# Kernel optimization log

Hardware: AMD Instinct MI355X
Metric: run time of the kernel (lower is better)

The kernel has to match this reference:

```python
import jax, jax.numpy as jnp
import numpy as np

B, N, E, H, D, FF = 4, 4096, 128, 8, 16, 512
EPS = 1e-6


def rmsnorm(x, w):
    return x * jax.lax.rsqrt(jnp.mean(x * x, axis=-1, keepdims=True) + EPS) * w


def setup_inputs() -> dict:
    key = jax.random.key(0)
    ks = jax.random.split(key, 12)
    s = 1.0 / np.sqrt(E)
    return {
        "x": jax.random.normal(ks[0], (B, N, E), jnp.float32),
        "dis_matrix": jax.random.uniform(ks[1], (B, N, N), jnp.float32),
        "g_in": jnp.ones((E,), jnp.float32),
        "g_post": jnp.ones((E,), jnp.float32),
        "Wq": jax.random.normal(ks[2], (E, E), jnp.float32) * s,
        "Wk": jax.random.normal(ks[3], (E, E), jnp.float32) * s,
        "Wv": jax.random.normal(ks[4], (E, E), jnp.float32) * s,
        "alpha": jnp.float32(1.0),
        "Wo": jax.random.normal(ks[5], (H * D, E), jnp.float32) * s,
        "W1": jax.random.normal(ks[6], (E, FF), jnp.float32) * s,
        "b1": jnp.zeros((FF,), jnp.float32),
        "W2": jax.random.normal(ks[7], (FF, E), jnp.float32) / np.sqrt(FF),
        "b2": jnp.zeros((E,), jnp.float32),
    }


def reference(x, dis_matrix, g_in, g_post, Wq, Wk, Wv, alpha, Wo, W1, b1, W2, b2):
    b, n, e = x.shape
    h = rmsnorm(x, g_in)
    # project and split heads: [B,N,E] -> [B,H,N,D]
    def heads(y):
        return y.reshape(b, n, H, D).transpose(0, 2, 1, 3)
    q = heads(h @ Wq)
    k = heads(h @ Wk)
    v = heads(h @ Wv)
    # distance-decayed kernel weights [B,N,N]
    dis_w = jnp.exp(-alpha * np.log2(n) * dis_matrix)
    kw = jnp.exp(k)  # [B,H,N,D]
    w1 = jnp.einsum('bij,bhik->bhjk', dis_w, kw * v)
    w2 = jnp.einsum('bij,bhik->bhjk', dis_w, kw)
    att = jax.nn.sigmoid(q) * (w1 / w2)  # [B,H,N,D]
    att = att.transpose(0, 2, 1, 3).reshape(b, n, e)
    out1 = x + att @ Wo
    h2 = rmsnorm(out1, g_post)
    ff = jax.nn.relu(h2 @ W1 + b1) @ W2 + b2
    return out1 + ff
```

## Files before the change

### kernel.cpp

```cpp
#include <hip/hip_runtime.h>
#include <stdint.h>


typedef __attribute__((ext_vector_type(8))) short short8;
typedef __attribute__((ext_vector_type(4))) float f32x4;

__device__ __forceinline__ uint16_t f2bf(float f) {
    uint32_t u = __builtin_bit_cast(uint32_t, f);
    u += 0x7fffu + ((u >> 16) & 1u);
    return (uint16_t)(u >> 16);
}
__device__ __forceinline__ float bf2f(uint16_t h) {
    uint32_t u = ((uint32_t)h) << 16;
    return __builtin_bit_cast(float, u);
}
__device__ __forceinline__ f32x4 mfma16(short8 a, short8 b, f32x4 c) {
    return __builtin_amdgcn_mfma_f32_16x16x32_bf16(a, b, c, 0, 0, 0);
}

__global__ __launch_bounds__(256) void k_prep(
    const float* __restrict__ Wq, const float* __restrict__ Wk,
    const float* __restrict__ Wv, const float* __restrict__ Wo,
    const float* __restrict__ W1, const float* __restrict__ W2,
    uint16_t* __restrict__ wqkvT, uint16_t* __restrict__ woT,
    uint16_t* __restrict__ w1T, uint16_t* __restrict__ w2T) {
    int t = blockIdx.x * 256 + threadIdx.x;
    if (t < 49152) {
        int n = t >> 7, k = t & 127;
        const float* W = (n < 128) ? Wq : (n < 256) ? Wk : Wv;
        wqkvT[t] = f2bf(W[k * 128 + (n & 127)]);
    } else if (t < 65536) {
        int i = t - 49152; int e = i >> 7, d = i & 127;
        woT[i] = f2bf(Wo[d * 128 + e]);
    } else if (t < 131072) {
        int i = t - 65536; int f = i >> 7, e = i & 127;
        w1T[i] = f2bf(W1[e * 512 + f]);
    } else if (t < 196608) {
        int i = t - 131072; int e = i >> 9, f = i & 511;
        w2T[i] = f2bf(W2[f * 128 + e]);
    }
}

__global__ __launch_bounds__(256) void k_rms(
    const float* __restrict__ x, const float* __restrict__ g,
    uint16_t* __restrict__ o) {
    int row = blockIdx.x * 4 + (threadIdx.x >> 6);
    int l = threadIdx.x & 63;
    float2 v = *(const float2*)(x + (size_t)row * 128 + l * 2);
    float ss = v.x * v.x + v.y * v.y;
    #pragma unroll
    for (int m = 32; m >= 1; m >>= 1) ss += __shfl_xor(ss, m, 64);
    float rs = rsqrtf(ss * (1.0f / 128.0f) + 1e-6f);
    float2 gv = *(const float2*)(g + l * 2);
    uint32_t lo = (uint32_t)f2bf(v.x * rs * gv.x) |
                  ((uint32_t)f2bf(v.y * rs * gv.y) << 16);
    *(uint32_t*)(o + (size_t)row * 128 + l * 2) = lo;
}

__global__ __launch_bounds__(384) void k_qkv(
    const uint16_t* __restrict__ h, const uint16_t* __restrict__ wqkvT,
    uint16_t* __restrict__ sigq, uint16_t* __restrict__ mcatT) {
    __shared__ __align__(16) char sm[65536];
    uint16_t* Al = (uint16_t*)sm;
    float*    Pl = (float*)sm;
    const int t = threadIdx.x;
    const int i0 = blockIdx.x * 64;
    for (int idx = t; idx < 1024; idx += 384) {
        int row = idx >> 4, c8 = (idx & 15) * 8;
        *(uint4*)&Al[row * 136 + c8] =
            *(const uint4*)(h + (size_t)(i0 + row) * 128 + c8);
    }
    __syncthreads();
    const int w = t >> 6, l = t & 63, ml = l & 15, qd = l >> 4;
    f32x4 acc[4][4];
    f32x4 zv = {0.f, 0.f, 0.f, 0.f};
    #pragma unroll
    for (int a = 0; a < 4; ++a)
        #pragma unroll
        for (int b = 0; b < 4; ++b) acc[a][b] = zv;
    #pragma unroll
    for (int kc = 0; kc < 4; ++kc) {
        short8 af[4], bfr[4];
        #pragma unroll
        for (int fm = 0; fm < 4; ++fm)
            af[fm] = *(const short8*)&Al[(fm * 16 + ml) * 136 + kc * 32 + qd * 8];
        #pragma unroll
        for (int fn = 0; fn < 4; ++fn)
            bfr[fn] = *(const short8*)(wqkvT + (w * 64 + fn * 16 + ml) * 128 + kc * 32 + qd * 8);
        #pragma unroll
        for (int fm = 0; fm < 4; ++fm)
            #pragma unroll
            for (int fn = 0; fn < 4; ++fn)
                acc[fm][fn] = mfma16(af[fm], bfr[fn], acc[fm][fn]);
    }
    __syncthreads();
    const int bb = i0 >> 12, il0 = i0 & 4095;
    if (w < 2) {
        #pragma unroll
        for (int fm = 0; fm < 4; ++fm)
            #pragma unroll
            for (int fn = 0; fn < 4; ++fn)
                #pragma unroll
                for (int r = 0; r < 4; ++r) {
                    int row = fm * 16 + qd * 4 + r;
                    int col = w * 64 + fn * 16 + ml;
                    sigq[(size_t)(i0 + row) * 128 + col] =
                        f2bf(1.f / (1.f + __expf(-acc[fm][fn][r])));
                }
    } else {
        int half = (w < 4) ? 0 : 1;
        int cbase = (w - (half ? 4 : 2)) * 64;
        #pragma unroll
        for (int fm = 0; fm < 4; ++fm)
            #pragma unroll
            for (int fn = 0; fn < 4; ++fn)
                #pragma unroll
                for (int r = 0; r < 4; ++r) {
                    int row = fm * 16 + qd * 4 + r;
                    int col = cbase + fn * 16 + ml;
                    float vv = acc[fm][fn][r];
                    if (!half) vv = __expf(vv);
                    Pl[row * 256 + half * 128 + ((col + row) & 127)] = vv;
                }
    }
    __syncthreads();
    for (int idx = t; idx < 16384; idx += 384) {
        int cc = idx >> 6, il = idx & 63;
        int pc = ((cc & 127) + il) & 127;
        float ekw = Pl[il * 256 + pc];
        float val = (cc < 128) ? ekw * Pl[il * 256 + 128 + pc] : ekw;
        mcatT[((size_t)bb * 256 + cc) * 4096 + il0 + il] = f2bf(val);
    }
}

__global__ __launch_bounds__(512) void k_big(
    const float* __restrict__ dis, const uint16_t* __restrict__ mcatT,
    const float* __restrict__ alpha_p, float* __restrict__ wbuf) {
    __shared__ __align__(16) uint16_t Al[128 * 72];
    __shared__ __align__(16) uint16_t Bl[256 * 72];
    const int t = threadIdx.x;
    const int j0 = blockIdx.x * 128;
    const int b  = blockIdx.y;
    const int sp = blockIdx.z;
    const float c = -12.0f * alpha_p[0];
    const int w = t >> 6, l = t & 63, ml = l & 15, qd = l >> 4;
    const int wm = w >> 2, wn = w & 3;
    const int sj4 = (t & 31) * 4, si0 = (t >> 5) * 4;
    const float* disb = dis + (size_t)b * 4096 * 4096;
    const uint16_t* mb = mcatT + (size_t)b * 256 * 4096;

    f32x4 acc[4][4];
    f32x4 zv = {0.f, 0.f, 0.f, 0.f};
    #pragma unroll
    for (int a = 0; a < 4; ++a)
        #pragma unroll
        for (int q = 0; q < 4; ++q) acc[a][q] = zv;

    for (int ks = 0; ks < 32; ++ks) {
        const int ig = sp * 2048 + ks * 64;
        float dv[4][4];
        #pragma unroll
        for (int r = 0; r < 4; ++r) {
            float4 v = *(const float4*)(disb + (size_t)(ig + si0 + r) * 4096 + j0 + sj4);
            dv[r][0] = v.x; dv[r][1] = v.y; dv[r][2] = v.z; dv[r][3] = v.w;
        }
        __syncthreads();
        #pragma unroll
        for (int jj = 0; jj < 4; ++jj) {
            uint32_t lo = (uint32_t)f2bf(__expf(c * dv[0][jj])) |
                          ((uint32_t)f2bf(__expf(c * dv[1][jj])) << 16);
            uint32_t hi = (uint32_t)f2bf(__expf(c * dv[2][jj])) |
                          ((uint32_t)f2bf(__expf(c * dv[3][jj])) << 16);
            uint2 pk = {lo, hi};
            *(uint2*)&Al[(sj4 + jj) * 72 + si0] = pk;
        }
        #pragma unroll
        for (int ii = 0; ii < 4; ++ii) {
            int idx = t + ii * 512;
            int row = idx >> 3, c8 = (idx & 7) * 8;
            *(uint4*)&Bl[row * 72 + c8] =
                *(const uint4*)(mb + (size_t)row * 4096 + ig + c8);
        }
        __syncthreads();
        #pragma unroll
        for (int kc = 0; kc < 2; ++kc) {
            short8 af[4], bfr[4];
            #pragma unroll
            for (int fm = 0; fm < 4; ++fm)
                af[fm] = *(const short8*)&Al[(wm * 64 + fm * 16 + ml) * 72 + kc * 32 + qd * 8];
            #pragma unroll
            for (int fn = 0; fn < 4; ++fn)
                bfr[fn] = *(const short8*)&Bl[(wn * 64 + fn * 16 + ml) * 72 + kc * 32 + qd * 8];
            #pragma unroll
            for (int fm = 0; fm < 4; ++fm)
                #pragma unroll
                for (int fn = 0; fn < 4; ++fn)
                    acc[fm][fn] = mfma16(af[fm], bfr[fn], acc[fm][fn]);
        }
    }
    float* ob = wbuf + ((size_t)(sp * 4 + b) * 4096 + j0) * 256;
    #pragma unroll
    for (int fm = 0; fm < 4; ++fm)
        #pragma unroll
        for (int fn = 0; fn < 4; ++fn) {
            int col = wn * 64 + fn * 16 + ml;
            #pragma unroll
            for (int r = 0; r < 4; ++r) {
                int rowl = wm * 64 + fm * 16 + qd * 4 + r;
                ob[(size_t)rowl * 256 + col] = acc[fm][fn][r];
            }
        }
}

__global__ __launch_bounds__(256) void k_att(
    const float* __restrict__ wbuf, const uint16_t* __restrict__ sigq,
    const uint16_t* __restrict__ woT, const float* __restrict__ x,
    float* __restrict__ out1) {
    __shared__ __align__(16) uint16_t Al[64 * 136];
    __shared__ __align__(16) uint16_t Bl[128 * 136];
    const int t = threadIdx.x;
    const int i0 = blockIdx.x * 64;
    const int b = i0 >> 12, jl0 = i0 & 4095;
    const float* wb0 = wbuf + ((size_t)b * 4096 + jl0) * 256;
    const float* wb1 = wbuf + ((size_t)(4 + b) * 4096 + jl0) * 256;
    #pragma unroll
    for (int ii = 0; ii < 8; ++ii) {
        int idx = t + ii * 256;
        int row = idx >> 5, c4 = (idx & 31) * 4;
        float4 a0 = *(const float4*)(wb0 + (size_t)row * 256 + c4);
        float4 a1 = *(const float4*)(wb1 + (size_t)row * 256 + c4);
        float4 d0 = *(const float4*)(wb0 + (size_t)row * 256 + 128 + c4);
        float4 d1 = *(const float4*)(wb1 + (size_t)row * 256 + 128 + c4);
        const uint16_t* sq = sigq + (size_t)(i0 + row) * 128 + c4;
        uint32_t lo = (uint32_t)f2bf(bf2f(sq[0]) * (a0.x + a1.x) / (d0.x + d1.x)) |
                      ((uint32_t)f2bf(bf2f(sq[1]) * (a0.y + a1.y) / (d0.y + d1.y)) << 16);
        uint32_t hi = (uint32_t)f2bf(bf2f(sq[2]) * (a0.z + a1.z) / (d0.z + d1.z)) |
                      ((uint32_t)f2bf(bf2f(sq[3]) * (a0.w + a1.w) / (d0.w + d1.w)) << 16);
        uint2 pk = {lo, hi};
        *(uint2*)&Al[row * 136 + c4] = pk;
    }
    #pragma unroll
    for (int ii = 0; ii < 8; ++ii) {
        int idx = t + ii * 256;
        int row = idx >> 4, c8 = (idx & 15) * 8;
        *(uint4*)&Bl[row * 136 + c8] = *(const uint4*)(woT + row * 128 + c8);
    }
    __syncthreads();
    const int w = t >> 6, l = t & 63, ml = l & 15, qd = l >> 4;
    const int wm = w >> 1, wn = w & 1;
    f32x4 acc[2][4];
    f32x4 zv = {0.f, 0.f, 0.f, 0.f};
    #pragma unroll
    for (int a = 0; a < 2; ++a)
        #pragma unroll
        for (int q = 0; q < 4; ++q) acc[a][q] = zv;
    #pragma unroll
    for (int kc = 0; kc < 4; ++kc) {
        short8 af[2], bfr[4];
        #pragma unroll
        for (int fm = 0; fm < 2; ++fm)
            af[fm] = *(const short8*)&Al[(wm * 32 + fm * 16 + ml) * 136 + kc * 32 + qd * 8];
        #pragma unroll
        for (int fn = 0; fn < 4; ++fn)
            bfr[fn] = *(const short8*)&Bl[(wn * 64 + fn * 16 + ml) * 136 + kc * 32 + qd * 8];
        #pragma unroll
        for (int fm = 0; fm < 2; ++fm)
            #pragma unroll
            for (int fn = 0; fn < 4; ++fn)
                acc[fm][fn] = mfma16(af[fm], bfr[fn], acc[fm][fn]);
    }
    #pragma unroll
    for (int fm = 0; fm < 2; ++fm)
        #pragma unroll
        for (int fn = 0; fn < 4; ++fn) {
            int col = wn * 64 + fn * 16 + ml;
            #pragma unroll
            for (int r = 0; r < 4; ++r) {
                int rowl = wm * 32 + fm * 16 + qd * 4 + r;
                size_t o = (size_t)(i0 + rowl) * 128 + col;
                out1[o] = x[o] + acc[fm][fn][r];
            }
        }
}

__global__ __launch_bounds__(256) void k_ff1(
    const uint16_t* __restrict__ h2, const uint16_t* __restrict__ w1T,
    const float* __restrict__ b1, uint16_t* __restrict__ R) {
    __shared__ __align__(16) uint16_t Al[64 * 136];
    __shared__ __align__(16) uint16_t Bl[128 * 136];
    const int t = threadIdx.x;
    const int i0 = blockIdx.x * 64;
    const int nt = blockIdx.y;
    #pragma unroll
    for (int ii = 0; ii < 4; ++ii) {
        int idx = t + ii * 256;
        int row = idx >> 4, c8 = (idx & 15) * 8;
        *(uint4*)&Al[row * 136 + c8] =
            *(const uint4*)(h2 + (size_t)(i0 + row) * 128 + c8);
    }
    #pragma unroll
    for (int ii = 0; ii < 8; ++ii) {
        int idx = t + ii * 256;
        int row = idx >> 4, c8 = (idx & 15) * 8;
        *(uint4*)&Bl[row * 136 + c8] =
            *(const uint4*)(w1T + (size_t)(nt * 128 + row) * 128 + c8);
    }
    __syncthreads();
    const int w = t >> 6, l = t & 63, ml = l & 15, qd = l >> 4;
    const int wm = w >> 1, wn = w & 1;
    f32x4 acc[2][4];
    f32x4 zv = {0.f, 0.f, 0.f, 0.f};
    #pragma unroll
    for (int a = 0; a < 2; ++a)
        #pragma unroll
        for (int q = 0; q < 4; ++q) acc[a][q] = zv;
    #pragma unroll
    for (int kc = 0; kc < 4; ++kc) {
        short8 af[2], bfr[4];
        #pragma unroll
        for (int fm = 0; fm < 2; ++fm)
            af[fm] = *(const short8*)&Al[(wm * 32 + fm * 16 + ml) * 136 + kc * 32 + qd * 8];
        #pragma unroll
        for (int fn = 0; fn < 4; ++fn)
            bfr[fn] = *(const short8*)&Bl[(wn * 64 + fn * 16 + ml) * 136 + kc * 32 + qd * 8];
        #pragma unroll
        for (int fm = 0; fm < 2; ++fm)
            #pragma unroll
            for (int fn = 0; fn < 4; ++fn)
                acc[fm][fn] = mfma16(af[fm], bfr[fn], acc[fm][fn]);
    }
    #pragma unroll
    for (int fm = 0; fm < 2; ++fm)
        #pragma unroll
        for (int fn = 0; fn < 4; ++fn) {
            int col = wn * 64 + fn * 16 + ml;
            int gcol = nt * 128 + col;
            #pragma unroll
            for (int r = 0; r < 4; ++r) {
                int rowl = wm * 32 + fm * 16 + qd * 4 + r;
                R[(size_t)(i0 + rowl) * 512 + gcol] =
                    f2bf(fmaxf(acc[fm][fn][r] + b1[gcol], 0.f));
            }
        }
}

__global__ __launch_bounds__(256) void k_ff2(
    const uint16_t* __restrict__ Rm, const uint16_t* __restrict__ w2T,
    const float* __restrict__ b2, const float* __restrict__ out1,
    float* __restrict__ out) {
    __shared__ __align__(16) uint16_t Al[64 * 136];
    __shared__ __align__(16) uint16_t Bl[128 * 136];
    const int t = threadIdx.x;
    const int i0 = blockIdx.x * 64;
    const int w = t >> 6, l = t & 63, ml = l & 15, qd = l >> 4;
    const int wm = w >> 1, wn = w & 1;
    f32x4 acc[2][4];
    f32x4 zv = {0.f, 0.f, 0.f, 0.f};
    #pragma unroll
    for (int a = 0; a < 2; ++a)
        #pragma unroll
        for (int q = 0; q < 4; ++q) acc[a][q] = zv;
    for (int kb = 0; kb < 4; ++kb) {
        __syncthreads();
        #pragma unroll
        for (int ii = 0; ii < 4; ++ii) {
            int idx = t + ii * 256;
            int row = idx >> 4, c8 = (idx & 15) * 8;
            *(uint4*)&Al[row * 136 + c8] =
                *(const uint4*)(Rm + (size_t)(i0 + row) * 512 + kb * 128 + c8);
        }
        #pragma unroll
        for (int ii = 0; ii < 8; ++ii) {
            int idx = t + ii * 256;
            int row = idx >> 4, c8 = (idx & 15) * 8;
            *(uint4*)&Bl[row * 136 + c8] =
                *(const uint4*)(w2T + (size_t)row * 512 + kb * 128 + c8);
        }
        __syncthreads();
        #pragma unroll
        for (int kc = 0; kc < 4; ++kc) {
            short8 af[2], bfr[4];
            #pragma unroll
            for (int fm = 0; fm < 2; ++fm)
                af[fm] = *(const short8*)&Al[(wm * 32 + fm * 16 + ml) * 136 + kc * 32 + qd * 8];
            #pragma unroll
            for (int fn = 0; fn < 4; ++fn)
                bfr[fn] = *(const short8*)&Bl[(wn * 64 + fn * 16 + ml) * 136 + kc * 32 + qd * 8];
            #pragma unroll
            for (int fm = 0; fm < 2; ++fm)
                #pragma unroll
                for (int fn = 0; fn < 4; ++fn)
                    acc[fm][fn] = mfma16(af[fm], bfr[fn], acc[fm][fn]);
        }
    }
    #pragma unroll
    for (int fm = 0; fm < 2; ++fm)
        #pragma unroll
        for (int fn = 0; fn < 4; ++fn) {
            int col = wn * 64 + fn * 16 + ml;
            #pragma unroll
            for (int r = 0; r < 4; ++r) {
                int rowl = wm * 32 + fm * 16 + qd * 4 + r;
                size_t o = (size_t)(i0 + rowl) * 128 + col;
                out[o] = out1[o] + b2[col] + acc[fm][fn][r];
            }
        }
}

extern "C" void kernel_launch(void* const* d_in, const int* in_sizes, int n_in,
                              void* d_out, int out_size, void* d_ws, size_t ws_size,
                              hipStream_t stream) {
    (void)in_sizes; (void)n_in; (void)out_size; (void)ws_size;
    const float* x      = (const float*)d_in[0];
    const float* dis    = (const float*)d_in[1];
    const float* g_in   = (const float*)d_in[2];
    const float* g_post = (const float*)d_in[3];
    const float* Wq     = (const float*)d_in[4];
    const float* Wk     = (const float*)d_in[5];
    const float* Wv     = (const float*)d_in[6];
    const float* alpha  = (const float*)d_in[7];
    const float* Wo     = (const float*)d_in[8];
    const float* W1     = (const float*)d_in[9];
    const float* b1     = (const float*)d_in[10];
    const float* W2     = (const float*)d_in[11];
    const float* b2     = (const float*)d_in[12];
    float* out = (float*)d_out;

    char* ws = (char*)d_ws;
    size_t off = 0;
    auto take = [&](size_t bytes) -> char* {
        char* p = ws + off;
        off += (bytes + 255) & ~(size_t)255;
        return p;
    };
    uint16_t* h     = (uint16_t*)take(16384ull * 128 * 2);
    uint16_t* wqkvT = (uint16_t*)take(384ull * 128 * 2);
    uint16_t* woT   = (uint16_t*)take(128ull * 128 * 2);
    uint16_t* w1T   = (uint16_t*)take(512ull * 128 * 2);
    uint16_t* w2T   = (uint16_t*)take(128ull * 512 * 2);
    uint16_t* sigq  = (uint16_t*)take(16384ull * 128 * 2);
    uint16_t* mcatT = (uint16_t*)take(4ull * 256 * 4096 * 2);
    float*    wbuf  = (float*)take(2ull * 4 * 4096 * 256 * 4);
    float*    out1  = (float*)take(16384ull * 128 * 4);
    uint16_t* h2    = (uint16_t*)take(16384ull * 128 * 2);
    uint16_t* R     = (uint16_t*)take(16384ull * 512 * 2);

    k_prep<<<768, 256, 0, stream>>>(Wq, Wk, Wv, Wo, W1, W2, wqkvT, woT, w1T, w2T);
    k_rms<<<4096, 256, 0, stream>>>(x, g_in, h);
    k_qkv<<<256, 384, 0, stream>>>(h, wqkvT, sigq, mcatT);
    k_big<<<dim3(32, 4, 2), 512, 0, stream>>>(dis, mcatT, alpha, wbuf);
    k_att<<<256, 256, 0, stream>>>(wbuf, sigq, woT, x, out1);
    k_rms<<<4096, 256, 0, stream>>>(out1, g_post, h2);
    k_ff1<<<dim3(256, 4), 256, 0, stream>>>(h2, w1T, b1, R);
    k_ff2<<<256, 256, 0, stream>>>(R, w2T, b2, out1, out);
}
```

Measured before the change: 467.3 us.

## Fuse prep kernels and tail stages, halve k_big tile with register prefetch

Merges weight conversion with the input RMSnorm into one launch. Fuses the attention output projection, post-norm, FF1 and FF2 into a single tail kernel that keeps intermediates in shared memory, removing the out1, h2 and R round trips through global memory. It also shrinks the k_big j-tile to 64 to launch twice as many blocks, adds register prefetch of the next dis and mcat tiles, and vectorises the mcatT stores in k_qkv. In exchange, the tail kernel reads weights straight from global memory per wave and uses about 58 KB of shared memory per block, which can limit occupancy.

Measured after the change: 530.4 us. +13.5%, slower.

```diff
diff --git a/kernel.cpp b/kernel.cpp
--- a/kernel.cpp
+++ b/kernel.cpp
@@ -18,43 +18,43 @@
     return __builtin_amdgcn_mfma_f32_16x16x32_bf16(a, b, c, 0, 0, 0);
 }
 
-__global__ __launch_bounds__(256) void k_prep(
+__global__ __launch_bounds__(256) void k_pre(
+    const float* __restrict__ x, const float* __restrict__ g_in,
     const float* __restrict__ Wq, const float* __restrict__ Wk,
     const float* __restrict__ Wv, const float* __restrict__ Wo,
     const float* __restrict__ W1, const float* __restrict__ W2,
-    uint16_t* __restrict__ wqkvT, uint16_t* __restrict__ woT,
-    uint16_t* __restrict__ w1T, uint16_t* __restrict__ w2T) {
-    int t = blockIdx.x * 256 + threadIdx.x;
-    if (t < 49152) {
-        int n = t >> 7, k = t & 127;
-        const float* W = (n < 128) ? Wq : (n < 256) ? Wk : Wv;
-        wqkvT[t] = f2bf(W[k * 128 + (n & 127)]);
-    } else if (t < 65536) {
-        int i = t - 49152; int e = i >> 7, d = i & 127;
-        woT[i] = f2bf(Wo[d * 128 + e]);
-    } else if (t < 131072) {
-        int i = t - 65536; int f = i >> 7, e = i & 127;
-        w1T[i] = f2bf(W1[e * 512 + f]);
-    } else if (t < 196608) {
-        int i = t - 131072; int e = i >> 9, f = i & 511;
-        w2T[i] = f2bf(W2[f * 128 + e]);
-    }
-}
-
-__global__ __launch_bounds__(256) void k_rms(
-    const float* __restrict__ x, const float* __restrict__ g,
-    uint16_t* __restrict__ o) {
-    int row = blockIdx.x * 4 + (threadIdx.x >> 6);
-    int l = threadIdx.x & 63;
-    float2 v = *(const float2*)(x + (size_t)row * 128 + l * 2);
-    float ss = v.x * v.x + v.y * v.y;
-    #pragma unroll
-    for (int m = 32; m >= 1; m >>= 1) ss += __shfl_xor(ss, m, 64);
-    float rs = rsqrtf(ss * (1.0f / 128.0f) + 1e-6f);
-    float2 gv = *(const float2*)(g + l * 2);
-    uint32_t lo = (uint32_t)f2bf(v.x * rs * gv.x) |
-                  ((uint32_t)f2bf(v.y * rs * gv.y) << 16);
-    *(uint32_t*)(o + (size_t)row * 128 + l * 2) = lo;
+    uint16_t* __restrict__ h, uint16_t* __restrict__ wqkvT,
+    uint16_t* __restrict__ woT, uint16_t* __restrict__ w1T,
+    uint16_t* __restrict__ w2T) {
+    if (blockIdx.x < 4096) {
+        int row = blockIdx.x * 4 + (threadIdx.x >> 6);
+        int l = threadIdx.x & 63;
+        float2 v = *(const float2*)(x + (size_t)row * 128 + l * 2);
+        float ss = v.x * v.x + v.y * v.y;
+        #pragma unroll
+        for (int m = 32; m >= 1; m >>= 1) ss += __shfl_xor(ss, m, 64);
+        float rs = rsqrtf(ss * (1.0f / 128.0f) + 1e-6f);
+        float2 gv = *(const float2*)(g_in + l * 2);
+        uint32_t lo = (uint32_t)f2bf(v.x * rs * gv.x) |
+                      ((uint32_t)f2bf(v.y * rs * gv.y) << 16);
+        *(uint32_t*)(h + (size_t)row * 128 + l * 2) = lo;
+    } else {
+        int t = (blockIdx.x - 4096) * 256 + threadIdx.x;
+        if (t < 49152) {
+            int n = t >> 7, k = t & 127;
+            const float* W = (n < 128) ? Wq : (n < 256) ? Wk : Wv;
+            wqkvT[t] = f2bf(W[k * 128 + (n & 127)]);
+        } else if (t < 65536) {
+            int i = t - 49152; int e = i >> 7, d = i & 127;
+            woT[i] = f2bf(Wo[d * 128 + e]);
+        } else if (t < 131072) {
+            int i = t - 65536; int f = i >> 7, e = i & 127;
+            w1T[i] = f2bf(W1[e * 512 + f]);
+        } else if (t < 196608) {
+            int i = t - 131072; int e = i >> 9, f = i & 511;
+            w2T[i] = f2bf(W2[f * 128 + e]);
+        }
+    }
 }
 
 __global__ __launch_bounds__(384) void k_qkv(
@@ -124,75 +124,93 @@
                 }
     }
     __syncthreads();
-    for (int idx = t; idx < 16384; idx += 384) {
-        int cc = idx >> 6, il = idx & 63;
-        int pc = ((cc & 127) + il) & 127;
-        float ekw = Pl[il * 256 + pc];
-        float val = (cc < 128) ? ekw * Pl[il * 256 + 128 + pc] : ekw;
-        mcatT[((size_t)bb * 256 + cc) * 4096 + il0 + il] = f2bf(val);
-    }
-}
-
-__global__ __launch_bounds__(512) void k_big(
+    for (int idx = t; idx < 4096; idx += 384) {
+        int cc = idx >> 4, il4 = (idx & 15) * 4;
+        float val[4];
+        #pragma unroll
+        for (int jj = 0; jj < 4; ++jj) {
+            int il = il4 + jj;
+            int pc = ((cc & 127) + il) & 127;
+            float ekw = Pl[il * 256 + pc];
+            val[jj] = (cc < 128) ? ekw * Pl[il * 256 + 128 + pc] : ekw;
+        }
+        uint2 pk;
+        pk.x = (uint32_t)f2bf(val[0]) | ((uint32_t)f2bf(val[1]) << 16);
+        pk.y = (uint32_t)f2bf(val[2]) | ((uint32_t)f2bf(val[3]) << 16);
+        *(uint2*)&mcatT[((size_t)bb * 256 + cc) * 4096 + il0 + il4] = pk;
+    }
+}
+
+__global__ __launch_bounds__(512, 4) void k_big(
     const float* __restrict__ dis, const uint16_t* __restrict__ mcatT,
     const float* __restrict__ alpha_p, float* __restrict__ wbuf) {
-    __shared__ __align__(16) uint16_t Al[128 * 72];
+    __shared__ __align__(16) uint16_t Al[64 * 72];
     __shared__ __align__(16) uint16_t Bl[256 * 72];
     const int t = threadIdx.x;
-    const int j0 = blockIdx.x * 128;
+    const int j0 = blockIdx.x * 64;
     const int b  = blockIdx.y;
     const int sp = blockIdx.z;
     const float c = -12.0f * alpha_p[0];
     const int w = t >> 6, l = t & 63, ml = l & 15, qd = l >> 4;
     const int wm = w >> 2, wn = w & 3;
-    const int sj4 = (t & 31) * 4, si0 = (t >> 5) * 4;
+    const int sj4 = (t & 15) * 4, si2 = (t >> 4) * 2;
+    const int brow = t >> 3, bc8 = (t & 7) * 8;
     const float* disb = dis + (size_t)b * 4096 * 4096;
     const uint16_t* mb = mcatT + (size_t)b * 256 * 4096;
-
-    f32x4 acc[4][4];
+    const int ig0 = sp * 2048;
+
+    f32x4 acc[2][4];
     f32x4 zv = {0.f, 0.f, 0.f, 0.f};
     #pragma unroll
-    for (int a = 0; a < 4; ++a)
+    for (int a = 0; a < 2; ++a)
         #pragma unroll
         for (int q = 0; q < 4; ++q) acc[a][q] = zv;
 
+    float4 da[2];
+    uint4  bv[4];
+    {
+        #pragma unroll
+        for (int r = 0; r < 2; ++r)
+            da[r] = *(const float4*)(disb + (size_t)(ig0 + si2 + r) * 4096 + j0 + sj4);
+        #pragma unroll
+        for (int ii = 0; ii < 4; ++ii)
+            bv[ii] = *(const uint4*)(mb + (size_t)(brow + ii * 64) * 4096 + ig0 + bc8);
+    }
+
     for (int ks = 0; ks < 32; ++ks) {
-        const int ig = sp * 2048 + ks * 64;
-        float dv[4][4];
-        #pragma unroll
-        for (int r = 0; r < 4; ++r) {
-            float4 v = *(const float4*)(disb + (size_t)(ig + si0 + r) * 4096 + j0 + sj4);
-            dv[r][0] = v.x; dv[r][1] = v.y; dv[r][2] = v.z; dv[r][3] = v.w;
-        }
         __syncthreads();
-        #pragma unroll
-        for (int jj = 0; jj < 4; ++jj) {
-            uint32_t lo = (uint32_t)f2bf(__expf(c * dv[0][jj])) |
-                          ((uint32_t)f2bf(__expf(c * dv[1][jj])) << 16);
-            uint32_t hi = (uint32_t)f2bf(__expf(c * dv[2][jj])) |
-                          ((uint32_t)f2bf(__expf(c * dv[3][jj])) << 16);
-            uint2 pk = {lo, hi};
-            *(uint2*)&Al[(sj4 + jj) * 72 + si0] = pk;
-        }
-        #pragma unroll
-        for (int ii = 0; ii < 4; ++ii) {
-            int idx = t + ii * 512;
-            int row = idx >> 3, c8 = (idx & 7) * 8;
-            *(uint4*)&Bl[row * 72 + c8] =
-                *(const uint4*)(mb + (size_t)row * 4096 + ig + c8);
+        float e00 = __expf(c * da[0].x), e01 = __expf(c * da[0].y);
+        float e02 = __expf(c * da[0].z), e03 = __expf(c * da[0].w);
+        float e10 = __expf(c * da[1].x), e11 = __expf(c * da[1].y);
+        float e12 = __expf(c * da[1].z), e13 = __expf(c * da[1].w);
+        *(uint32_t*)&Al[(sj4 + 0) * 72 + si2] = (uint32_t)f2bf(e00) | ((uint32_t)f2bf(e10) << 16);
+        *(uint32_t*)&Al[(sj4 + 1) * 72 + si2] = (uint32_t)f2bf(e01) | ((uint32_t)f2bf(e11) << 16);
+        *(uint32_t*)&Al[(sj4 + 2) * 72 + si2] = (uint32_t)f2bf(e02) | ((uint32_t)f2bf(e12) << 16);
+        *(uint32_t*)&Al[(sj4 + 3) * 72 + si2] = (uint32_t)f2bf(e03) | ((uint32_t)f2bf(e13) << 16);
+        #pragma unroll
+        for (int ii = 0; ii < 4; ++ii)
+            *(uint4*)&Bl[(brow + ii * 64) * 72 + bc8] = bv[ii];
+        if (ks + 1 < 32) {
+            const int ig = ig0 + (ks + 1) * 64;
+            #pragma unroll
+            for (int r = 0; r < 2; ++r)
+                da[r] = *(const float4*)(disb + (size_t)(ig + si2 + r) * 4096 + j0 + sj4);
+            #pragma unroll
+            for (int ii = 0; ii < 4; ++ii)
+                bv[ii] = *(const uint4*)(mb + (size_t)(brow + ii * 64) * 4096 + ig + bc8);
         }
         __syncthreads();
         #pragma unroll
         for (int kc = 0; kc < 2; ++kc) {
-            short8 af[4], bfr[4];
-            #pragma unroll
-            for (int fm = 0; fm < 4; ++fm)
-                af[fm] = *(const short8*)&Al[(wm * 64 + fm * 16 + ml) * 72 + kc * 32 + qd * 8];
+            short8 af[2], bfr[4];
+            #pragma unroll
+            for (int fm = 0; fm < 2; ++fm)
+                af[fm] = *(const short8*)&Al[(wm * 32 + fm * 16 + ml) * 72 + kc * 32 + qd * 8];
             #pragma unroll
             for (int fn = 0; fn < 4; ++fn)
                 bfr[fn] = *(const short8*)&Bl[(wn * 64 + fn * 16 + ml) * 72 + kc * 32 + qd * 8];
             #pragma unroll
-            for (int fm = 0; fm < 4; ++fm)
+            for (int fm = 0; fm < 2; ++fm)
                 #pragma unroll
                 for (int fn = 0; fn < 4; ++fn)
                     acc[fm][fn] = mfma16(af[fm], bfr[fn], acc[fm][fn]);
@@ -200,211 +218,177 @@
     }
     float* ob = wbuf + ((size_t)(sp * 4 + b) * 4096 + j0) * 256;
     #pragma unroll
-    for (int fm = 0; fm < 4; ++fm)
+    for (int fm = 0; fm < 2; ++fm)
         #pragma unroll
         for (int fn = 0; fn < 4; ++fn) {
             int col = wn * 64 + fn * 16 + ml;
             #pragma unroll
             for (int r = 0; r < 4; ++r) {
-                int rowl = wm * 64 + fm * 16 + qd * 4 + r;
+                int rowl = wm * 32 + fm * 16 + qd * 4 + r;
                 ob[(size_t)rowl * 256 + col] = acc[fm][fn][r];
             }
         }
 }
 
-__global__ __launch_bounds__(256) void k_att(
+__global__ __launch_bounds__(256, 3) void k_tail(
     const float* __restrict__ wbuf, const uint16_t* __restrict__ sigq,
     const uint16_t* __restrict__ woT, const float* __restrict__ x,
-    float* __restrict__ out1) {
-    __shared__ __align__(16) uint16_t Al[64 * 136];
-    __shared__ __align__(16) uint16_t Bl[128 * 136];
+    const float* __restrict__ g_post, const uint16_t* __restrict__ w1T,
+    const float* __restrict__ b1, const uint16_t* __restrict__ w2T,
+    const float* __restrict__ b2, float* __restrict__ out) {
+    __shared__ __align__(16) char sm[58880];
+    uint16_t* Rl  = (uint16_t*)sm;
+    float*    O1l = (float*)(sm + 33280);
+    uint16_t* AHl = (uint16_t*)(sm + 50176);
     const int t = threadIdx.x;
-    const int i0 = blockIdx.x * 64;
+    const int i0 = blockIdx.x * 32;
     const int b = i0 >> 12, jl0 = i0 & 4095;
     const float* wb0 = wbuf + ((size_t)b * 4096 + jl0) * 256;
     const float* wb1 = wbuf + ((size_t)(4 + b) * 4096 + jl0) * 256;
     #pragma unroll
-    for (int ii = 0; ii < 8; ++ii) {
+    for (int ii = 0; ii < 4; ++ii) {
         int idx = t + ii * 256;
         int row = idx >> 5, c4 = (idx & 31) * 4;
         float4 a0 = *(const float4*)(wb0 + (size_t)row * 256 + c4);
         float4 a1 = *(const float4*)(wb1 + (size_t)row * 256 + c4);
         float4 d0 = *(const float4*)(wb0 + (size_t)row * 256 + 128 + c4);
         float4 d1 = *(const float4*)(wb1 + (size_t)row * 256 + 128 + c4);
-        const uint16_t* sq = sigq + (size_t)(i0 + row) * 128 + c4;
-        uint32_t lo = (uint32_t)f2bf(bf2f(sq[0]) * (a0.x + a1.x) / (d0.x + d1.x)) |
-                      ((uint32_t)f2bf(bf2f(sq[1]) * (a0.y + a1.y) / (d0.y + d1.y)) << 16);
-        uint32_t hi = (uint32_t)f2bf(bf2f(sq[2]) * (a0.z + a1.z) / (d0.z + d1.z)) |
-                      ((uint32_t)f2bf(bf2f(sq[3]) * (a0.w + a1.w) / (d0.w + d1.w)) << 16);
-        uint2 pk = {lo, hi};
-        *(uint2*)&Al[row * 136 + c4] = pk;
-    }
-    #pragma unroll
-    for (int ii = 0; ii < 8; ++ii) {
-        int idx = t + ii * 256;
-        int row = idx >> 4, c8 = (idx & 15) * 8;
-        *(uint4*)&Bl[row * 136 + c8] = *(const uint4*)(woT + row * 128 + c8);
+        uint2 sq = *(const uint2*)(sigq + (size_t)(i0 + row) * 128 + c4);
+        uint2 pk;
+        pk.x = (uint32_t)f2bf(bf2f((uint16_t)sq.x) * (a0.x + a1.x) / (d0.x + d1.x)) |
+               ((uint32_t)f2bf(bf2f((uint16_t)(sq.x >> 16)) * (a0.y + a1.y) / (d0.y + d1.y)) << 16);
+        pk.y = (uint32_t)f2bf(bf2f((uint16_t)sq.y) * (a0.z + a1.z) / (d0.z + d1.z)) |
+               ((uint32_t)f2bf(bf2f((uint16_t)(sq.y >> 16)) * (a0.w + a1.w) / (d0.w + d1.w)) << 16);
+        *(uint2*)&AHl[row * 136 + c4] = pk;
     }
     __syncthreads();
     const int w = t >> 6, l = t & 63, ml = l & 15, qd = l >> 4;
-    const int wm = w >> 1, wn = w & 1;
-    f32x4 acc[2][4];
     f32x4 zv = {0.f, 0.f, 0.f, 0.f};
-    #pragma unroll
-    for (int a = 0; a < 2; ++a)
-        #pragma unroll
-        for (int q = 0; q < 4; ++q) acc[a][q] = zv;
-    #pragma unroll
-    for (int kc = 0; kc < 4; ++kc) {
-        short8 af[2], bfr[4];
+    {
+        f32x4 acc[2][2];
+        #pragma unroll
+        for (int a = 0; a < 2; ++a) { acc[a][0] = zv; acc[a][1] = zv; }
+        #pragma unroll
+        for (int kc = 0; kc < 4; ++kc) {
+            short8 af[2], bfr[2];
+            #pragma unroll
+            for (int fm = 0; fm < 2; ++fm)
+                af[fm] = *(const short8*)&AHl[(fm * 16 + ml) * 136 + kc * 32 + qd * 8];
+            #pragma unroll
+            for (int fn = 0; fn < 2; ++fn)
+                bfr[fn] = *(const short8*)(woT + (size_t)(w * 32 + fn * 16 + ml) * 128 + kc * 32 + qd * 8);
+            #pragma unroll
+            for (int fm = 0; fm < 2; ++fm)
+                #pragma unroll
+                for (int fn = 0; fn < 2; ++fn)
+                    acc[fm][fn] = mfma16(af[fm], bfr[fn], acc[fm][fn]);
+        }
         #pragma unroll
         for (int fm = 0; fm < 2; ++fm)
-            af[fm] = *(const short8*)&Al[(wm * 32 + fm * 16 + ml) * 136 + kc * 32 + qd * 8];
-        #pragma unroll
-        for (int fn = 0; fn < 4; ++fn)
-            bfr[fn] = *(const short8*)&Bl[(wn * 64 + fn * 16 + ml) * 136 + kc * 32 + qd * 8];
+            #pragma unroll
+            for (int fn = 0; fn < 2; ++fn) {
+                int col = w * 32 + fn * 16 + ml;
+                #pragma unroll
+                for (int r = 0; r < 4; ++r) {
+                    int rowl = fm * 16 + qd * 4 + r;
+                    O1l[rowl * 132 + col] =
+                        x[(size_t)(i0 + rowl) * 128 + col] + acc[fm][fn][r];
+                }
+            }
+    }
+    __syncthreads();
+    {
+        int row = t >> 3, seg = t & 7;
+        float vb[16];
+        float ss = 0.f;
+        #pragma unroll
+        for (int cq = 0; cq < 4; ++cq) {
+            float4 v = *(const float4*)&O1l[row * 132 + seg * 16 + cq * 4];
+            vb[cq * 4 + 0] = v.x; vb[cq * 4 + 1] = v.y;
+            vb[cq * 4 + 2] = v.z; vb[cq * 4 + 3] = v.w;
+            ss += v.x * v.x + v.y * v.y + v.z * v.z + v.w * v.w;
+        }
+        ss += __shfl_xor(ss, 1, 64);
+        ss += __shfl_xor(ss, 2, 64);
+        ss += __shfl_xor(ss, 4, 64);
+        float rs = rsqrtf(ss * (1.0f / 128.0f) + 1e-6f);
+        #pragma unroll
+        for (int cp = 0; cp < 8; ++cp) {
+            float2 gv = *(const float2*)(g_post + seg * 16 + cp * 2);
+            uint32_t p = (uint32_t)f2bf(vb[cp * 2] * rs * gv.x) |
+                         ((uint32_t)f2bf(vb[cp * 2 + 1] * rs * gv.y) << 16);
+            *(uint32_t*)&AHl[row * 136 + seg * 16 + cp * 2] = p;
+        }
+    }
+    __syncthreads();
+    {
+        f32x4 acc[2][8];
+        #pragma unroll
+        for (int a = 0; a < 2; ++a)
+            #pragma unroll
+            for (int q = 0; q < 8; ++q) acc[a][q] = zv;
+        #pragma unroll
+        for (int kc = 0; kc < 4; ++kc) {
+            short8 af[2], bfr[8];
+            #pragma unroll
+            for (int fm = 0; fm < 2; ++fm)
+                af[fm] = *(const short8*)&AHl[(fm * 16 + ml) * 136 + kc * 32 + qd * 8];
+            #pragma unroll
+            for (int fn = 0; fn < 8; ++fn)
+                bfr[fn] = *(const short8*)(w1T + (size_t)(w * 128 + fn * 16 + ml) * 128 + kc * 32 + qd * 8);
+            #pragma unroll
+            for (int fm = 0; fm < 2; ++fm)
+                #pragma unroll
+                for (int fn = 0; fn < 8; ++fn)
+                    acc[fm][fn] = mfma16(af[fm], bfr[fn], acc[fm][fn]);
+        }
         #pragma unroll
         for (int fm = 0; fm < 2; ++fm)
             #pragma unroll
-            for (int fn = 0; fn < 4; ++fn)
-                acc[fm][fn] = mfma16(af[fm], bfr[fn], acc[fm][fn]);
-    }
-    #pragma unroll
-    for (int fm = 0; fm < 2; ++fm)
-        #pragma unroll
-        for (int fn = 0; fn < 4; ++fn) {
-            int col = wn * 64 + fn * 16 + ml;
-            #pragma unroll
-            for (int r = 0; r < 4; ++r) {
-                int rowl = wm * 32 + fm * 16 + qd * 4 + r;
-                size_t o = (size_t)(i0 + rowl) * 128 + col;
-                out1[o] = x[o] + acc[fm][fn][r];
+            for (int fn = 0; fn < 8; ++fn) {
+                int gcol = w * 128 + fn * 16 + ml;
+                float bv = b1[gcol];
+                #pragma unroll
+                for (int r = 0; r < 4; ++r) {
+                    int rowl = fm * 16 + qd * 4 + r;
+                    Rl[rowl * 520 + gcol] = f2bf(fmaxf(acc[fm][fn][r] + bv, 0.f));
+                }
             }
-        }
-}
-
-__global__ __launch_bounds__(256) void k_ff1(
-    const uint16_t* __restrict__ h2, const uint16_t* __restrict__ w1T,
-    const float* __restrict__ b1, uint16_t* __restrict__ R) {
-    __shared__ __align__(16) uint16_t Al[64 * 136];
-    __shared__ __align__(16) uint16_t Bl[128 * 136];
-    const int t = threadIdx.x;
-    const int i0 = blockIdx.x * 64;
-    const int nt = blockIdx.y;
-    #pragma unroll
-    for (int ii = 0; ii < 4; ++ii) {
-        int idx = t + ii * 256;
-        int row = idx >> 4, c8 = (idx & 15) * 8;
-        *(uint4*)&Al[row * 136 + c8] =
-            *(const uint4*)(h2 + (size_t)(i0 + row) * 128 + c8);
-    }
-    #pragma unroll
-    for (int ii = 0; ii < 8; ++ii) {
-        int idx = t + ii * 256;
-        int row = idx >> 4, c8 = (idx & 15) * 8;
-        *(uint4*)&Bl[row * 136 + c8] =
-            *(const uint4*)(w1T + (size_t)(nt * 128 + row) * 128 + c8);
-    }
-    __syncthreads();
-    const int w = t >> 6, l = t & 63, ml = l & 15, qd = l >> 4;
-    const int wm = w >> 1, wn = w & 1;
-    f32x4 acc[2][4];
-    f32x4 zv = {0.f, 0.f, 0.f, 0.f};
-    #pragma unroll
-    for (int a = 0; a < 2; ++a)
-        #pragma unroll
-        for (int q = 0; q < 4; ++q) acc[a][q] = zv;
-    #pragma unroll
-    for (int kc = 0; kc < 4; ++kc) {
-        short8 af[2], bfr[4];
+    }
+    __syncthreads();
+    {
+        f32x4 acc[2][2];
+        #pragma unroll
+        for (int a = 0; a < 2; ++a) { acc[a][0] = zv; acc[a][1] = zv; }
+        #pragma unroll
+        for (int kc = 0; kc < 16; ++kc) {
+            short8 af[2], bfr[2];
+            #pragma unroll
+            for (int fm = 0; fm < 2; ++fm)
+                af[fm] = *(const short8*)&Rl[(fm * 16 + ml) * 520 + kc * 32 + qd * 8];
+            #pragma unroll
+            for (int fn = 0; fn < 2; ++fn)
+                bfr[fn] = *(const short8*)(w2T + (size_t)(w * 32 + fn * 16 + ml) * 512 + kc * 32 + qd * 8);
+            #pragma unroll
+            for (int fm = 0; fm < 2; ++fm)
+                #pragma unroll
+                for (int fn = 0; fn < 2; ++fn)
+                    acc[fm][fn] = mfma16(af[fm], bfr[fn], acc[fm][fn]);
+        }
         #pragma unroll
         for (int fm = 0; fm < 2; ++fm)
-            af[fm] = *(const short8*)&Al[(wm * 32 + fm * 16 + ml) * 136 + kc * 32 + qd * 8];
-        #pragma unroll
-        for (int fn = 0; fn < 4; ++fn)
-            bfr[fn] = *(const short8*)&Bl[(wn * 64 + fn * 16 + ml) * 136 + kc * 32 + qd * 8];
-        #pragma unroll
-        for (int fm = 0; fm < 2; ++fm)
-            #pragma unroll
-            for (int fn = 0; fn < 4; ++fn)
-                acc[fm][fn] = mfma16(af[fm], bfr[fn], acc[fm][fn]);
-    }
-    #pragma unroll
-    for (int fm = 0; fm < 2; ++fm)
-        #pragma unroll
-        for (int fn = 0; fn < 4; ++fn) {
-            int col = wn * 64 + fn * 16 + ml;
-            int gcol = nt * 128 + col;
-            #pragma unroll
-            for (int r = 0; r < 4; ++r) {
-                int rowl = wm * 32 + fm * 16 + qd * 4 + r;
-                R[(size_t)(i0 + rowl) * 512 + gcol] =
-                    f2bf(fmaxf(acc[fm][fn][r] + b1[gcol], 0.f));
+            #pragma unroll
+            for (int fn = 0; fn < 2; ++fn) {
+                int col = w * 32 + fn * 16 + ml;
+                float bv = b2[col];
+                #pragma unroll
+                for (int r = 0; r < 4; ++r) {
+                    int rowl = fm * 16 + qd * 4 + r;
+                    out[(size_t)(i0 + rowl) * 128 + col] =
+                        O1l[rowl * 132 + col] + bv + acc[fm][fn][r];
+                }
             }
-        }
-}
-
-__global__ __launch_bounds__(256) void k_ff2(
-    const uint16_t* __restrict__ Rm, const uint16_t* __restrict__ w2T,
-    const float* __restrict__ b2, const float* __restrict__ out1,
-    float* __restrict__ out) {
-    __shared__ __align__(16) uint16_t Al[64 * 136];
-    __shared__ __align__(16) uint16_t Bl[128 * 136];
-    const int t = threadIdx.x;
-    const int i0 = blockIdx.x * 64;
-    const int w = t >> 6, l = t & 63, ml = l & 15, qd = l >> 4;
-    const int wm = w >> 1, wn = w & 1;
-    f32x4 acc[2][4];
-    f32x4 zv = {0.f, 0.f, 0.f, 0.f};
-    #pragma unroll
-    for (int a = 0; a < 2; ++a)
-        #pragma unroll
-        for (int q = 0; q < 4; ++q) acc[a][q] = zv;
-    for (int kb = 0; kb < 4; ++kb) {
-        __syncthreads();
-        #pragma unroll
-        for (int ii = 0; ii < 4; ++ii) {
-            int idx = t + ii * 256;
-            int row = idx >> 4, c8 = (idx & 15) * 8;
-            *(uint4*)&Al[row * 136 + c8] =
-                *(const uint4*)(Rm + (size_t)(i0 + row) * 512 + kb * 128 + c8);
-        }
-        #pragma unroll
-        for (int ii = 0; ii < 8; ++ii) {
-            int idx = t + ii * 256;
-            int row = idx >> 4, c8 = (idx & 15) * 8;
-            *(uint4*)&Bl[row * 136 + c8] =
-                *(const uint4*)(w2T + (size_t)row * 512 + kb * 128 + c8);
-        }
-        __syncthreads();
-        #pragma unroll
-        for (int kc = 0; kc < 4; ++kc) {
-            short8 af[2], bfr[4];
-            #pragma unroll
-            for (int fm = 0; fm < 2; ++fm)
-                af[fm] = *(const short8*)&Al[(wm * 32 + fm * 16 + ml) * 136 + kc * 32 + qd * 8];
-            #pragma unroll
-            for (int fn = 0; fn < 4; ++fn)
-                bfr[fn] = *(const short8*)&Bl[(wn * 64 + fn * 16 + ml) * 136 + kc * 32 + qd * 8];
-            #pragma unroll
-            for (int fm = 0; fm < 2; ++fm)
-                #pragma unroll
-                for (int fn = 0; fn < 4; ++fn)
-                    acc[fm][fn] = mfma16(af[fm], bfr[fn], acc[fm][fn]);
-        }
-    }
-    #pragma unroll
-    for (int fm = 0; fm < 2; ++fm)
-        #pragma unroll
-        for (int fn = 0; fn < 4; ++fn) {
-            int col = wn * 64 + fn * 16 + ml;
-            #pragma unroll
-            for (int r = 0; r < 4; ++r) {
-                int rowl = wm * 32 + fm * 16 + qd * 4 + r;
-                size_t o = (size_t)(i0 + rowl) * 128 + col;
-                out[o] = out1[o] + b2[col] + acc[fm][fn][r];
-            }
-        }
+    }
 }
 
 extern "C" void kernel_launch(void* const* d_in, const int* in_sizes, int n_in,
@@ -441,16 +425,10 @@
     uint16_t* sigq  = (uint16_t*)take(16384ull * 128 * 2);
     uint16_t* mcatT = (uint16_t*)take(4ull * 256 * 4096 * 2);
     float*    wbuf  = (float*)take(2ull * 4 * 4096 * 256 * 4);
-    float*    out1  = (float*)take(16384ull * 128 * 4);
-    uint16_t* h2    = (uint16_t*)take(16384ull * 128 * 2);
-    uint16_t* R     = (uint16_t*)take(16384ull * 512 * 2);
-
-    k_prep<<<768, 256, 0, stream>>>(Wq, Wk, Wv, Wo, W1, W2, wqkvT, woT, w1T, w2T);
-    k_rms<<<4096, 256, 0, stream>>>(x, g_in, h);
+
+    k_pre<<<4864, 256, 0, stream>>>(x, g_in, Wq, Wk, Wv, Wo, W1, W2,
+                                    h, wqkvT, woT, w1T, w2T);
     k_qkv<<<256, 384, 0, stream>>>(h, wqkvT, sigq, mcatT);
-    k_big<<<dim3(32, 4, 2), 512, 0, stream>>>(dis, mcatT, alpha, wbuf);
-    k_att<<<256, 256, 0, stream>>>(wbuf, sigq, woT, x, out1);
-    k_rms<<<4096, 256, 0, stream>>>(out1, g_post, h2);
-    k_ff1<<<dim3(256, 4), 256, 0, stream>>>(h2, w1T, b1, R);
-    k_ff2<<<256, 256, 0, stream>>>(R, w2T, b2, out1, out);
-}
+    k_big<<<dim3(64, 4, 2), 512, 0, stream>>>(dis, mcatT, alpha, wbuf);
+    k_tail<<<512, 256, 0, stream>>>(wbuf, sigq, woT, x, g_post, w1T, b1, w2T, b2, out);
+}
```
